# Kernel tuning notes

Measured on AMD Instinct MI355X. Metric: run time of the kernel, lower is better.

The kernel has to match this reference:

```python
import jax, jax.numpy as jnp
import numpy as np

N, B = 1024, 32
PEP_PAD, L, M, E, VOCAB = 3, 27, 34, 16, 26
CN, KS, OFFS = (128, 256, 256), (3, 5, 7), (2, 1, 0)
LIN = (512, 256)
BN_EPS = 1e-5


def _pe(length, d):
    pos = np.arange(length, dtype=np.float32)[:, None]
    div = np.exp(np.arange(0, d, 2, dtype=np.float32) * (-np.log(10000.0) / d))
    pe = np.zeros((length, d), np.float32)
    pe[:, 0::2] = np.sin(pos * div)
    pe[:, 1::2] = np.cos(pos * div)
    return jnp.asarray(pe)

PE_MHC = _pe(M, E)
PE_PEP = _pe(100, E)[: L - 2 * PEP_PAD]


def _bn(x, g, b):
    # inference-mode BatchNorm2d (running_mean=0, running_var=1)
    s = g / jnp.sqrt(1.0 + BN_EPS)
    return x * s[None, :, None, None] + b[None, :, None, None]


def _iconv(pep, mhc, W, b):
    # interaction conv: pep (N, Lin, E, S), mhc (N, M, E), W (C, K, M)
    # out[n,c,i,s] = sum_{k,m,e} W[c,k,m] * mhc[n,m,e] * pep[n,i+k,e,s] + b[c]
    K = W.shape[1]
    Kb = jnp.einsum('ckm,nme->ncke', W, mhc)  # per-sample kernel (N,C,K,E)
    Lout = pep.shape[1] - K + 1
    out = sum(jnp.einsum('nce,nies->ncis', Kb[:, :, k], pep[:, k:k + Lout]) for k in range(K))
    return out + b[None, :, None, None]


def _fwd(params, peptide_x, mhc_x, bags_size, inverse):
    (emb_pep, emb_mhc, convs_f, convs_r, lins_f, lins_r,
     w_att1, b_att1, w_att2, b_att2, w_out, b_out) = params
    masks = peptide_x[:, PEP_PAD:L - PEP_PAD] != 0              # (N, 21)
    mhc_e = emb_mhc[mhc_x] + PE_MHC                             # (N, 34, E)
    pep_e = emb_pep[peptide_x]
    pep_e = jnp.concatenate([pep_e[:, :PEP_PAD],
                             pep_e[:, PEP_PAD:L - PEP_PAD] + PE_PEP,
                             pep_e[:, L - PEP_PAD:]], axis=1)    # (N, 27, E)
    pep_c = pep_e[..., None]                                     # (N,27,E,1)
    pep_i = jnp.stack([pep_e[:, ::-1], pep_e], axis=-1)          # (N,27,E,2)

    def branch(pep, convs, inversion):
        outs = []
        for (W, bb, g, be), off in zip(convs, OFFS):
            Wk = W[:, ::-1] if inversion else W
            x = _iconv(pep[:, off:L - off], mhc_e, Wk, bb)
            outs.append(jax.nn.relu(_bn(x, g, be)))
        return jnp.concatenate(outs, axis=1)

    conv_out = branch(pep_c, convs_f, False)                     # (N, 640, 21, 1)
    conv_r = branch(pep_i, convs_r, True)                        # (N, 640, 21, 2)
    conv_r = jnp.concatenate([conv_r[..., 0:1][:, :, ::-1], conv_r[..., 1:2]], axis=-1)

    def mlp(x, lins):
        for Wl, bl, gl, bel in lins:
            x = jax.nn.relu(_bn(jnp.einsum('oc,nciw->noiw', Wl, x) + bl[None, :, None, None], gl, bel))
        return x

    conv_out = mlp(conv_out, lins_f)                             # (N, 256, 21, 1)
    conv_r = mlp(conv_r, lins_r)                                 # (N, 256, 21, 2)
    x = jnp.concatenate([conv_out, conv_r], axis=-1)             # (N, 256, 21, 3)
    m = masks[:, None, -x.shape[2]:, None]
    pool = jnp.max(jnp.where(m, x, -jnp.inf), axis=2, keepdims=True)  # (N,256,1,3)

    # attention MIL over variable-size bags (segment softmax)
    feat = pool.mean(axis=(2, 3))                                # (N, 256)
    a = (jnp.tanh(feat @ w_att1.T + b_att1) @ w_att2.T + b_att2)[:, 0]
    nb = bags_size.shape[0]
    seg = jnp.repeat(jnp.arange(nb), bags_size, total_repeat_length=feat.shape[0])
    amax = jax.lax.stop_gradient(jax.ops.segment_max(a, seg, num_segments=nb))
    ex = jnp.exp(a - amax[seg])
    att = ex / jax.ops.segment_sum(ex, seg, num_segments=nb)[seg]

    score = jax.nn.sigmoid(jnp.einsum('oc,nciw->noiw', w_out, pool) + b_out[None, :, None, None])  # (N,2,1,3)
    half = score[..., :2].sum(-1) * 0.5
    if inverse:
        s = jnp.stack([half, score[..., -1]], axis=-1)           # (N,2,1,2)
    else:
        s = jnp.stack([half, half], axis=-1)
    s = s.max(axis=-1)                                           # (N, 2, 1)
    if inverse:
        s = jax.ops.segment_sum(att[:, None, None] * s, seg, num_segments=nb)  # (B,2,1)
    else:
        s = s.sum(axis=-1) * 0.5
    s = jnp.clip(s, 0.0, 1.0)
    return s.reshape(s.shape[0], -1)                             # (B, 2)


def setup_inputs() -> dict:
    key = jax.random.key(0)
    ks = iter(jax.random.split(key, 64))
    nrm = lambda shape, std=0.02: jax.random.normal(next(ks), shape, jnp.float32) * std
    d = {}
    d['peptide_x'] = jax.random.randint(next(ks), (N, L), 1, VOCAB)
    d['mhc_x'] = jax.random.randint(next(ks), (N, M), 1, VOCAB)
    d['context_x'] = jax.random.randint(next(ks), (N, 12), 1, VOCAB)
    d['peptide_esm_x'] = jnp.zeros((N, 2, 10, 3), jnp.float32)
    d['bags_size'] = jnp.full((B,), N // B, jnp.int32)
    d['inverse'] = 1
    d['emb_pep'] = jax.random.uniform(next(ks), (VOCAB, E), jnp.float32, -0.1, 0.1)
    d['emb_mhc'] = jax.random.uniform(next(ks), (VOCAB, E), jnp.float32, -0.1, 0.1)
    for tag in ('cf', 'cr'):
        for j, (c, k) in enumerate(zip(CN, KS)):
            d[f'w_{tag}{j}'] = nrm((c, k, M), 0.05)
            d[f'b_{tag}{j}'] = jnp.zeros((c,), jnp.float32)
            d[f'g_{tag}{j}'] = 1.0 + nrm((c,), 0.002)
            d[f'be_{tag}{j}'] = jnp.zeros((c,), jnp.float32)
    dims = [sum(CN)] + list(LIN)
    for tag in ('lf', 'lr'):
        for j, (i_s, o_s) in enumerate(zip(dims[:-1], dims[1:])):
            d[f'w_{tag}{j}'] = nrm((o_s, i_s), 0.02)
            d[f'b_{tag}{j}'] = jnp.zeros((o_s,), jnp.float32)
            d[f'g_{tag}{j}'] = 1.0 + nrm((o_s,), 0.002)
            d[f'be_{tag}{j}'] = jnp.zeros((o_s,), jnp.float32)
    H = LIN[-1]
    d['w_att1'] = nrm((H, H)); d['b_att1'] = jnp.zeros((H,), jnp.float32)
    d['w_att2'] = nrm((1, H)); d['b_att2'] = jnp.zeros((1,), jnp.float32)
    d['w_out'] = nrm((2, H), 0.1); d['b_out'] = jnp.zeros((2,), jnp.float32)
    return d


def reference(peptide_x, mhc_x, context_x, peptide_esm_x, bags_size, inverse,
              emb_pep, emb_mhc,
              w_cf0, b_cf0, g_cf0, be_cf0, w_cf1, b_cf1, g_cf1, be_cf1, w_cf2, b_cf2, g_cf2, be_cf2,
              w_cr0, b_cr0, g_cr0, be_cr0, w_cr1, b_cr1, g_cr1, be_cr1, w_cr2, b_cr2, g_cr2, be_cr2,
              w_lf0, b_lf0, g_lf0, be_lf0, w_lf1, b_lf1, g_lf1, be_lf1,
              w_lr0, b_lr0, g_lr0, be_lr0, w_lr1, b_lr1, g_lr1, be_lr1,
              w_att1, b_att1, w_att2, b_att2, w_out, b_out):
    convs_f = [(w_cf0, b_cf0, g_cf0, be_cf0), (w_cf1, b_cf1, g_cf1, be_cf1), (w_cf2, b_cf2, g_cf2, be_cf2)]
    convs_r = [(w_cr0, b_cr0, g_cr0, be_cr0), (w_cr1, b_cr1, g_cr1, be_cr1), (w_cr2, b_cr2, g_cr2, be_cr2)]
    lins_f = [(w_lf0, b_lf0, g_lf0, be_lf0), (w_lf1, b_lf1, g_lf1, be_lf1)]
    lins_r = [(w_lr0, b_lr0, g_lr0, be_lr0), (w_lr1, b_lr1, g_lr1, be_lr1)]
    params = (emb_pep, emb_mhc, convs_f, convs_r, lins_f, lins_r,
              w_att1, b_att1, w_att2, b_att2, w_out, b_out)
    return _fwd(params, peptide_x, mhc_x, bags_size, int(inverse))
```

## Files before the change

### kernel.cpp

```cpp
#include <hip/hip_runtime.h>
#include <hip/hip_bf16.h>
#include <math.h>

#define NS   1024
#define LP   27
#define MMH  34
#define EE   16
#define LO   21
#define CT   640
#define H1   512
#define H2   256
#define LPAD 40
#define GROW (LP*LPAD)
#define SLOTROWS (NS*LO)
#define ALLROWS  (3*SLOTROWS)

typedef __attribute__((ext_vector_type(8))) short  s8v;
typedef __attribute__((ext_vector_type(4))) float  f4v;

#define PK2_SLOT 147456
#define PK2_J0   0
#define PK2_J1   16384
#define PK2_J2   73728
#define WMLP_FAM 458752
#define WMLP_B   327680
#define BMLP_FAM 768
#define BMLP_B   512

__device__ __forceinline__ ushort f2b(float v) {
    __hip_bfloat16 hb = __float2bfloat16(v);
    return *reinterpret_cast<ushort*>(&hb);
}

__device__ __forceinline__ float pe_val(int pos, int e) {
    int j = e >> 1;
    float div = expf(-1.1512925464970229f * (float)j);
    float ang = (float)pos * div;
    return (e & 1) ? cosf(ang) : sinf(ang);
}

struct PrepArgs {
    const int* pep_x; const int* mhc_x;
    const float* emb_pep; const float* emb_mhc;
    const float* cw[2][3]; const float* cb[2][3]; const float* cg[2][3]; const float* cbe[2][3];
    const float* mw[4]; const float* mb[4]; const float* mg[4]; const float* mbe[4];
    ushort* Gb; ushort* Wpack; float* bpack; ushort* Wmlp; float* bmlp;
};

__global__ __launch_bounds__(256) void k_prep(PrepArgs A) {
    int b = blockIdx.x, t = threadIdx.x;
    float rs = rsqrtf(1.0f + 1e-5f);
    if (b < NS) {
        __shared__ float ps[LP * 17];
        __shared__ float ms[MMH * 17];
        int n = b;
        for (int idx = t; idx < LP * EE; idx += 256) {
            int l = idx >> 4, e = idx & 15;
            float v = A.emb_pep[A.pep_x[n * LP + l] * EE + e];
            if (l >= 3 && l < 24) v += pe_val(l - 3, e);
            ps[l * 17 + e] = v;
        }
        for (int idx = t; idx < MMH * EE; idx += 256) {
            int m = idx >> 4, e = idx & 15;
            ms[m * 17 + e] = A.emb_mhc[A.mhc_x[n * MMH + m] * EE + e] + pe_val(m, e);
        }
        __syncthreads();
        for (int idx = t; idx < GROW; idx += 256) {
            int l = idx / LPAD, m = idx - l * LPAD;
            float s = 0.f;
            if (m < MMH) {
                #pragma unroll
                for (int e = 0; e < EE; ++e) s = fmaf(ps[l * 17 + e], ms[m * 17 + e], s);
            }
            A.Gb[(size_t)n * GROW + idx] = f2b(s);
        }
        if (n == 0 && t < 64) A.Gb[(size_t)NS * GROW + t] = 0;
    } else if (b < NS + 144) {
        const int KS_[3]  = {3, 5, 7};
        const int KCP_[3] = {128, 224, 288};
        const int NC_[3]  = {128, 256, 256};
        const int pkoff[3] = {PK2_J0, PK2_J1, PK2_J2};
        const int bpoff[3] = {0, 128, 384};
        int lin = b - NS;
        int s = lin / 48, rem = lin - s * 48, j = rem >> 4, z = rem & 15;
        int K = KS_[j], Kcp = KCP_[j], nc = NC_[j];
        int fam = (s == 0) ? 0 : 1;
        const float* w  = A.cw[fam][j];
        const float* g  = A.cg[fam][j];
        ushort* Wp = A.Wpack + s * PK2_SLOT + pkoff[j];
        int tot = nc * Kcp;
        for (int idx = z * 256 + t; idx < tot; idx += 16 * 256) {
            int c = idx / Kcp, col = idx - c * Kcp;
            int k = col / LPAD, m = col - k * LPAD;
            float v = 0.f;
            if (k < K && m < MMH) {
                int kk = (s == 2) ? (K - 1 - k) : k;
                v = w[((size_t)c * K + kk) * MMH + m] * (g[c] * rs);
            }
            Wp[idx] = f2b(v);
        }
        if (z == 0) {
            const float* bb = A.cb[fam][j];
            const float* be = A.cbe[fam][j];
            float* bp = A.bpack + s * CT + bpoff[j];
            for (int c = t; c < nc; c += 256)
                bp[c] = bb[c] * (g[c] * rs) + be[c];
        }
    } else {
        int lin = b - NS - 144;
        int task, rel, nb;
        if (lin < 40)      { task = 0; rel = lin;      nb = 40; }
        else if (lin < 56) { task = 1; rel = lin - 40; nb = 16; }
        else if (lin < 96) { task = 2; rel = lin - 56; nb = 40; }
        else               { task = 3; rel = lin - 96; nb = 16; }
        int fam = task >> 1, stage = task & 1;
        int Co = stage ? H2 : H1;
        int Ci = stage ? H1 : CT;
        const float* w  = A.mw[task];
        const float* g  = A.mg[task];
        ushort* Wb = A.Wmlp + fam * WMLP_FAM + stage * WMLP_B;
        int tot = Co * Ci;
        for (int idx = rel * 256 + t; idx < tot; idx += nb * 256) {
            int o = idx / Ci;
            Wb[idx] = f2b(w[idx] * (g[o] * rs));
        }
        if (rel == 0) {
            const float* bb = A.mb[task];
            const float* be = A.mbe[task];
            float* bp = A.bmlp + fam * BMLP_FAM + stage * BMLP_B;
            for (int o = t; o < Co; o += 256)
                bp[o] = bb[o] * (g[o] * rs) + be[o];
        }
    }
}

__global__ __launch_bounds__(256) void k_cmfma(
    const ushort* __restrict__ Gb, const ushort* __restrict__ Wpack,
    const float* __restrict__ bpack, ushort* __restrict__ Xb, int rowBase)
{
    const int kcpm[5] = {128, 224, 224, 288, 288};
    const int offm[5] = {2, 1, 1, 0, 0};
    const int o0m[5]  = {0, 0, 128, 0, 128};
    const int c0m[5]  = {0, 128, 128, 384, 384};
    const int wofm[5] = {PK2_J0, PK2_J1, PK2_J1, PK2_J2, PK2_J2};

    __shared__ ushort Al[128 * 40];
    __shared__ ushort Bl[128 * 40];
    int y = blockIdx.y;
    int Kcp = kcpm[y], off = offm[y], o0 = o0m[y];
    int r0g = rowBase + blockIdx.x * 128;
    int slot = r0g / SLOTROWS;
    const ushort* Wt = Wpack + slot * PK2_SLOT + wofm[y] + (size_t)o0 * Kcp;
    const float*  bp = bpack + slot * CT;
    int p0 = r0g - rowBase;

    int t = threadIdx.x, lane = t & 63, w = t >> 6;
    int r0 = (w >> 1) * 64, c0w = (w & 1) * 64;

    int row_a = t >> 2, seg = t & 3;
    int rg0 = r0g + row_a, rg1 = rg0 + 64;
    int rr0 = rg0 - slot * SLOTROWS, rr1 = rg1 - slot * SLOTROWS;
    size_t wb0 = (size_t)(rr0 / LO) * GROW + (off + rr0 % LO) * LPAD;
    size_t wb1 = (size_t)(rr1 / LO) * GROW + (off + rr1 % LO) * LPAD;

    f4v acc[4][4];
    #pragma unroll
    for (int m = 0; m < 4; ++m)
        #pragma unroll
        for (int n = 0; n < 4; ++n)
            acc[m][n] = (f4v){0.f, 0.f, 0.f, 0.f};

    int nkt = Kcp >> 5;
    for (int kt = 0; kt < nkt; ++kt) {
        int k0 = kt << 5;
        __syncthreads();
        *(s8v*)&Al[row_a * 40 + seg * 8]        = *(const s8v*)&Gb[wb0 + k0 + seg * 8];
        *(s8v*)&Al[(row_a + 64) * 40 + seg * 8] = *(const s8v*)&Gb[wb1 + k0 + seg * 8];
        *(s8v*)&Bl[row_a * 40 + seg * 8]        = *(const s8v*)&Wt[(size_t)row_a * Kcp + k0 + seg * 8];
        *(s8v*)&Bl[(row_a + 64) * 40 + seg * 8] = *(const s8v*)&Wt[(size_t)(row_a + 64) * Kcp + k0 + seg * 8];
        __syncthreads();
        s8v a[4], b[4];
        #pragma unroll
        for (int m = 0; m < 4; ++m)
            a[m] = *(const s8v*)&Al[(r0 + m * 16 + (lane & 15)) * 40 + (lane >> 4) * 8];
        #pragma unroll
        for (int n = 0; n < 4; ++n)
            b[n] = *(const s8v*)&Bl[(c0w + n * 16 + (lane & 15)) * 40 + (lane >> 4) * 8];
        #pragma unroll
        for (int m = 0; m < 4; ++m)
            #pragma unroll
            for (int n = 0; n < 4; ++n)
                acc[m][n] = __builtin_amdgcn_mfma_f32_16x16x32_bf16(a[m], b[n], acc[m][n], 0, 0, 0);
    }

    int cl = lane & 15, rq = lane >> 4;
    #pragma unroll
    for (int m = 0; m < 4; ++m) {
        #pragma unroll
        for (int n = 0; n < 4; ++n) {
            int oc = c0m[y] + o0 + c0w + n * 16 + cl;
            float bv = bp[oc];
            #pragma unroll
            for (int j = 0; j < 4; ++j) {
                int p = p0 + r0 + m * 16 + rq * 4 + j;
                Xb[(size_t)p * CT + oc] = f2b(fmaxf(acc[m][n][j] + bv, 0.f));
            }
        }
    }
}

template<int OUTB>
__global__ __launch_bounds__(256) void k_mgemm(
    const ushort* __restrict__ Xin, int Cin,
    const ushort* __restrict__ Wbase, const float* __restrict__ bbase,
    int woff, int boff,
    ushort* __restrict__ Yb, float* __restrict__ Yf, int Cout, int rowBase)
{
    __shared__ ushort Al[128 * 40];
    __shared__ ushort Bl[128 * 40];
    int t = threadIdx.x;
    int p0g = rowBase + blockIdx.x * 128;
    int fam = (p0g < SLOTROWS) ? 0 : 1;
    const ushort* Wb = Wbase + (size_t)fam * WMLP_FAM + woff;
    const float*  bp = bbase + fam * BMLP_FAM + boff;
    int p0 = p0g - rowBase, o0 = blockIdx.y * 128;
    int lane = t & 63, w = t >> 6;
    int r0 = (w >> 1) * 64, c0 = (w & 1) * 64;

    f4v acc[4][4];
    #pragma unroll
    for (int m = 0; m < 4; ++m)
        #pragma unroll
        for (int n = 0; n < 4; ++n)
            acc[m][n] = (f4v){0.f, 0.f, 0.f, 0.f};

    int nkt = Cin >> 5;
    for (int kt = 0; kt < nkt; ++kt) {
        int k0 = kt << 5;
        __syncthreads();
        #pragma unroll
        for (int h = 0; h < 2; ++h) {
            int L = t + h * 256;
            int row = L >> 2, seg = L & 3;
            *(s8v*)&Al[row * 40 + seg * 8] =
                *(const s8v*)&Xin[(size_t)(p0 + row) * Cin + k0 + seg * 8];
            *(s8v*)&Bl[row * 40 + seg * 8] =
                *(const s8v*)&Wb[(size_t)(o0 + row) * Cin + k0 + seg * 8];
        }
        __syncthreads();
        s8v a[4], b[4];
        #pragma unroll
        for (int m = 0; m < 4; ++m)
            a[m] = *(const s8v*)&Al[(r0 + m * 16 + (lane & 15)) * 40 + (lane >> 4) * 8];
        #pragma unroll
        for (int n = 0; n < 4; ++n)
            b[n] = *(const s8v*)&Bl[(c0 + n * 16 + (lane & 15)) * 40 + (lane >> 4) * 8];
        #pragma unroll
        for (int m = 0; m < 4; ++m)
            #pragma unroll
            for (int n = 0; n < 4; ++n)
                acc[m][n] = __builtin_amdgcn_mfma_f32_16x16x32_bf16(a[m], b[n], acc[m][n], 0, 0, 0);
    }

    int cl = lane & 15, rq = lane >> 4;
    #pragma unroll
    for (int m = 0; m < 4; ++m) {
        #pragma unroll
        for (int n = 0; n < 4; ++n) {
            int o = o0 + c0 + n * 16 + cl;
            float bv = bp[o];
            #pragma unroll
            for (int j = 0; j < 4; ++j) {
                int p = p0 + r0 + m * 16 + rq * 4 + j;
                float v = fmaxf(acc[m][n][j] + bv, 0.f);
                if (OUTB) {
                    Yb[(size_t)p * Cout + o] = f2b(v);
                } else {
                    Yf[(size_t)p * Cout + o] = v;
                }
            }
        }
    }
}

__global__ __launch_bounds__(128) void k_pool(
    const float* __restrict__ Zc, const int* __restrict__ pep_x,
    float* __restrict__ pool, int rowBase)
{
    int sl = blockIdx.x;
    int sg = rowBase / LO + sl;
    int slot = sg / NS, n = sg - slot * NS;
    int c = blockIdx.y * 128 + threadIdx.x;
    float m = -INFINITY;
    for (int i = 0; i < LO; ++i)
        if (pep_x[n * LP + 3 + i] != 0)
            m = fmaxf(m, Zc[(size_t)(sl * LO + i) * H2 + c]);
    pool[(size_t)n * (3 * H2) + slot * H2 + c] = m;
}

__global__ __launch_bounds__(256) void k_poolhead(
    const float* __restrict__ pool,
    const float* __restrict__ w_att1, const float* __restrict__ b_att1,
    const float* __restrict__ w_att2, const float* __restrict__ b_att2,
    const float* __restrict__ w_out, const float* __restrict__ b_out,
    float* __restrict__ a_out, float* __restrict__ s2_out)
{
    int n = blockIdx.x, c = threadIdx.x;
    __shared__ float feat_s[H2];
    __shared__ float red[7][H2];
    __shared__ float sc_s[6];

    float mx[3];
    #pragma unroll
    for (int w = 0; w < 3; ++w)
        mx[w] = pool[(size_t)n * (3 * H2) + w * H2 + c];

    float fv = (mx[0] + mx[1] + mx[2]) * (1.f / 3.f);
    feat_s[c] = fv;
    #pragma unroll
    for (int o = 0; o < 2; ++o)
        #pragma unroll
        for (int w = 0; w < 3; ++w)
            red[o * 3 + w][c] = w_out[o * H2 + c] * mx[w];
    __syncthreads();

    float hacc = 0.f;
    for (int cc = 0; cc < H2; ++cc)
        hacc = fmaf(w_att1[(size_t)c * H2 + cc], feat_s[cc], hacc);
    float h = tanhf(hacc + b_att1[c]);
    red[6][c] = h * w_att2[c];
    __syncthreads();

    for (int s = 128; s > 0; s >>= 1) {
        if (c < s) {
            #pragma unroll
            for (int jj = 0; jj < 7; ++jj) red[jj][c] += red[jj][c + s];
        }
        __syncthreads();
    }
    if (c == 0) a_out[n] = red[6][0] + b_att2[0];
    if (c < 6) {
        float x = red[c][0] + b_out[c / 3];
        sc_s[c] = 1.f / (1.f + expf(-x));
    }
    __syncthreads();
    if (c < 2) {
        float half = 0.5f * (sc_s[c * 3 + 0] + sc_s[c * 3 + 1]);
        s2_out[n * 2 + c] = fmaxf(half, sc_s[c * 3 + 2]);
    }
}

__global__ __launch_bounds__(1024) void k_final(
    const float* __restrict__ a_in, const float* __restrict__ s2_in,
    const int* __restrict__ bags, float* __restrict__ out)
{
    __shared__ float a_s[NS], s0_s[NS], s1_s[NS];
    __shared__ int off_s[33];
    int t = threadIdx.x;
    a_s[t]  = a_in[t];
    s0_s[t] = s2_in[t * 2 + 0];
    s1_s[t] = s2_in[t * 2 + 1];
    if (t == 0) {
        off_s[0] = 0;
        for (int g = 0; g < 32; ++g) off_s[g + 1] = off_s[g] + bags[g];
    }
    __syncthreads();
    if (t < 32) {
        int st = off_s[t], en = off_s[t + 1];
        float mxv = -INFINITY;
        for (int n = st; n < en; ++n) mxv = fmaxf(mxv, a_s[n]);
        float se = 0.f;
        for (int n = st; n < en; ++n) se += expf(a_s[n] - mxv);
        float inv = 1.f / se;
        float o0 = 0.f, o1 = 0.f;
        for (int n = st; n < en; ++n) {
            float w = expf(a_s[n] - mxv) * inv;
            o0 += w * s0_s[n];
            o1 += w * s1_s[n];
        }
        out[t * 2 + 0] = fminf(fmaxf(o0, 0.f), 1.f);
        out[t * 2 + 1] = fminf(fmaxf(o1, 0.f), 1.f);
    }
}

extern "C" void kernel_launch(void* const* d_in, const int* in_sizes, int n_in,
                              void* d_out, int out_size, void* d_ws, size_t ws_size,
                              hipStream_t stream) {
    const int* pep_x = (const int*)d_in[0];
    const int* mhc_x = (const int*)d_in[1];
    const int* bags  = (const int*)d_in[4];

    char* wsb = (char*)d_ws;
    float*  pool   = (float*) (wsb + 0);
    float*  a_buf  = (float*) (wsb + 3145728);
    float*  s2_buf = (float*) (wsb + 3149824);
    ushort* Wpack  = (ushort*)(wsb + 3158016);
    float*  bpack  = (float*) (wsb + 4042752);
    ushort* Wmlp   = (ushort*)(wsb + 4050432);
    float*  bmlp   = (float*) (wsb + 5885440);
    ushort* Gb     = (ushort*)(wsb + 5891584);
    const size_t XB_B = 8103552;

    size_t fullNeed = XB_B + (size_t)ALLROWS * (1280 + 1024 + 1024);
    int chunkSlots = (fullNeed <= ws_size) ? 3 : 1;
    int RC = chunkSlots * SLOTROWS;
    ushort* Xb = (ushort*)(wsb + XB_B);
    ushort* Yb = (ushort*)((char*)Xb + (size_t)RC * 1280);
    float*  Zc = (float*) ((char*)Yb + (size_t)RC * 1024);

    PrepArgs pa;
    pa.pep_x = pep_x; pa.mhc_x = mhc_x;
    pa.emb_pep = (const float*)d_in[6];
    pa.emb_mhc = (const float*)d_in[7];
    for (int j = 0; j < 3; ++j) {
        pa.cw[0][j]  = (const float*)d_in[8 + 4 * j];
        pa.cb[0][j]  = (const float*)d_in[9 + 4 * j];
        pa.cg[0][j]  = (const float*)d_in[10 + 4 * j];
        pa.cbe[0][j] = (const float*)d_in[11 + 4 * j];
        pa.cw[1][j]  = (const float*)d_in[20 + 4 * j];
        pa.cb[1][j]  = (const float*)d_in[21 + 4 * j];
        pa.cg[1][j]  = (const float*)d_in[22 + 4 * j];
        pa.cbe[1][j] = (const float*)d_in[23 + 4 * j];
    }
    for (int task = 0; task < 4; ++task) {
        int base = 32 + task * 4;
        pa.mw[task]  = (const float*)d_in[base + 0];
        pa.mb[task]  = (const float*)d_in[base + 1];
        pa.mg[task]  = (const float*)d_in[base + 2];
        pa.mbe[task] = (const float*)d_in[base + 3];
    }
    pa.Gb = Gb; pa.Wpack = Wpack; pa.bpack = bpack; pa.Wmlp = Wmlp; pa.bmlp = bmlp;

    k_prep<<<dim3(NS + 144 + 112), dim3(256), 0, stream>>>(pa);

    for (int rowBase = 0; rowBase < ALLROWS; rowBase += RC) {
        int nRB = RC / 128;
        k_cmfma<<<dim3(nRB, 5), dim3(256), 0, stream>>>(Gb, Wpack, bpack, Xb, rowBase);
        k_mgemm<1><<<dim3(nRB, H1 / 128), dim3(256), 0, stream>>>(
            Xb, CT, Wmlp, bmlp, 0, 0, Yb, nullptr, H1, rowBase);
        k_mgemm<0><<<dim3(nRB, H2 / 128), dim3(256), 0, stream>>>(
            Yb, H1, Wmlp, bmlp, WMLP_B, BMLP_B, nullptr, Zc, H2, rowBase);
        k_pool<<<dim3(RC / LO, H2 / 128), dim3(128), 0, stream>>>(
            Zc, pep_x, pool, rowBase);
    }

    k_poolhead<<<dim3(NS), dim3(256), 0, stream>>>(
        pool,
        (const float*)d_in[48], (const float*)d_in[49], (const float*)d_in[50], (const float*)d_in[51],
        (const float*)d_in[52], (const float*)d_in[53],
        a_buf, s2_buf);

    k_final<<<dim3(1), dim3(1024), 0, stream>>>(a_buf, s2_buf, bags, (float*)d_out);
}
```

Baseline: 231.2 us.

## Fuse masked max-pool into second MLP GEMM and stage GEMM outputs through LDS

Drops the separate pooling kernel and the fp32 Zc intermediate. The second MLP GEMM now does a masked max over sequence positions in shared memory and combines partial maxima across row tiles with integer atomicMax into a pool buffer that k_prep zeroes. The conv and MLP GEMM epilogues stage results in LDS so global stores become 16-byte vectorized writes, and the MLP GEMMs use a K-tile of 64. The grid order is swapped so column tiles sharing an A row-tile run next to each other. The atomicMax trick only holds for non-negative ReLU outputs and adds atomics plus extra shared memory per block.

```diff
diff --git a/kernel.cpp b/kernel.cpp
--- a/kernel.cpp
+++ b/kernel.cpp
@@ -44,7 +44,7 @@
     const float* emb_pep; const float* emb_mhc;
     const float* cw[2][3]; const float* cb[2][3]; const float* cg[2][3]; const float* cbe[2][3];
     const float* mw[4]; const float* mb[4]; const float* mg[4]; const float* mbe[4];
-    ushort* Gb; ushort* Wpack; float* bpack; ushort* Wmlp; float* bmlp;
+    ushort* Gb; ushort* Wpack; float* bpack; ushort* Wmlp; float* bmlp; int* poolI;
 };
 
 __global__ __launch_bounds__(256) void k_prep(PrepArgs A) {
@@ -106,7 +106,7 @@
             for (int c = t; c < nc; c += 256)
                 bp[c] = bb[c] * (g[c] * rs) + be[c];
         }
-    } else {
+    } else if (b < NS + 144 + 112) {
         int lin = b - NS - 144;
         int task, rel, nb;
         if (lin < 40)      { task = 0; rel = lin;      nb = 40; }
@@ -131,6 +131,11 @@
             for (int o = t; o < Co; o += 256)
                 bp[o] = bb[o] * (g[o] * rs) + be[o];
         }
+    } else {
+        int base = (b - NS - 144 - 112) * 8192;
+        #pragma unroll
+        for (int q = 0; q < 32; ++q)
+            A.poolI[base + q * 256 + t] = 0;
     }
 }
 
@@ -144,15 +149,17 @@
     const int c0m[5]  = {0, 128, 128, 384, 384};
     const int wofm[5] = {PK2_J0, PK2_J1, PK2_J1, PK2_J2, PK2_J2};
 
-    __shared__ ushort Al[128 * 40];
-    __shared__ ushort Bl[128 * 40];
-    int y = blockIdx.y;
+    __shared__ ushort smC[17408];
+    ushort* Al = smC;
+    ushort* Bl = smC + 5120;
+    int y = blockIdx.x;
     int Kcp = kcpm[y], off = offm[y], o0 = o0m[y];
-    int r0g = rowBase + blockIdx.x * 128;
+    int c0X = c0m[y] + o0;
+    int r0g = rowBase + blockIdx.y * 128;
     int slot = r0g / SLOTROWS;
     const ushort* Wt = Wpack + slot * PK2_SLOT + wofm[y] + (size_t)o0 * Kcp;
     const float*  bp = bpack + slot * CT;
-    int p0 = r0g - rowBase;
+    int p0 = blockIdx.y * 128;
 
     int t = threadIdx.x, lane = t & 63, w = t >> 6;
     int r0 = (w >> 1) * 64, c0w = (w & 1) * 64;
@@ -194,36 +201,41 @@
     }
 
     int cl = lane & 15, rq = lane >> 4;
-    #pragma unroll
-    for (int m = 0; m < 4; ++m) {
+    __syncthreads();
+    #pragma unroll
+    for (int m = 0; m < 4; ++m)
         #pragma unroll
         for (int n = 0; n < 4; ++n) {
-            int oc = c0m[y] + o0 + c0w + n * 16 + cl;
-            float bv = bp[oc];
-            #pragma unroll
-            for (int j = 0; j < 4; ++j) {
-                int p = p0 + r0 + m * 16 + rq * 4 + j;
-                Xb[(size_t)p * CT + oc] = f2b(fmaxf(acc[m][n][j] + bv, 0.f));
-            }
-        }
-    }
-}
-
-template<int OUTB>
-__global__ __launch_bounds__(256) void k_mgemm(
-    const ushort* __restrict__ Xin, int Cin,
+            int ocr = c0w + n * 16 + cl;
+            float bv = bp[c0X + ocr];
+            #pragma unroll
+            for (int j = 0; j < 4; ++j)
+                smC[(r0 + m * 16 + rq * 4 + j) * 136 + ocr] = f2b(fmaxf(acc[m][n][j] + bv, 0.f));
+        }
+    __syncthreads();
+    int ci = t & 15;
+    #pragma unroll
+    for (int it = 0; it < 8; ++it) {
+        int row = (t >> 4) + it * 16;
+        *(s8v*)&Xb[(size_t)(p0 + row) * CT + c0X + ci * 8] = *(const s8v*)&smC[row * 136 + ci * 8];
+    }
+}
+
+__global__ __launch_bounds__(256) void k_mgemmA(
+    const ushort* __restrict__ Xin,
     const ushort* __restrict__ Wbase, const float* __restrict__ bbase,
-    int woff, int boff,
-    ushort* __restrict__ Yb, float* __restrict__ Yf, int Cout, int rowBase)
+    ushort* __restrict__ Yb, int rowBase)
 {
-    __shared__ ushort Al[128 * 40];
-    __shared__ ushort Bl[128 * 40];
+    __shared__ ushort smA[18432];
+    ushort* Al = smA;
+    ushort* Bl = smA + 9216;
     int t = threadIdx.x;
-    int p0g = rowBase + blockIdx.x * 128;
-    int fam = (p0g < SLOTROWS) ? 0 : 1;
-    const ushort* Wb = Wbase + (size_t)fam * WMLP_FAM + woff;
-    const float*  bp = bbase + fam * BMLP_FAM + boff;
-    int p0 = p0g - rowBase, o0 = blockIdx.y * 128;
+    int o0 = blockIdx.x * 128;
+    int p0 = blockIdx.y * 128;
+    int g0 = rowBase + p0;
+    int fam = (g0 < SLOTROWS) ? 0 : 1;
+    const ushort* Wb = Wbase + (size_t)fam * WMLP_FAM;
+    const float*  bp = bbase + fam * BMLP_FAM;
     int lane = t & 63, w = t >> 6;
     int r0 = (w >> 1) * 64, c0 = (w & 1) * 64;
 
@@ -234,68 +246,148 @@
         for (int n = 0; n < 4; ++n)
             acc[m][n] = (f4v){0.f, 0.f, 0.f, 0.f};
 
-    int nkt = Cin >> 5;
-    for (int kt = 0; kt < nkt; ++kt) {
-        int k0 = kt << 5;
-        __syncthreads();
-        #pragma unroll
-        for (int h = 0; h < 2; ++h) {
-            int L = t + h * 256;
-            int row = L >> 2, seg = L & 3;
-            *(s8v*)&Al[row * 40 + seg * 8] =
-                *(const s8v*)&Xin[(size_t)(p0 + row) * Cin + k0 + seg * 8];
-            *(s8v*)&Bl[row * 40 + seg * 8] =
-                *(const s8v*)&Wb[(size_t)(o0 + row) * Cin + k0 + seg * 8];
-        }
-        __syncthreads();
-        s8v a[4], b[4];
-        #pragma unroll
-        for (int m = 0; m < 4; ++m)
-            a[m] = *(const s8v*)&Al[(r0 + m * 16 + (lane & 15)) * 40 + (lane >> 4) * 8];
+    for (int kt = 0; kt < CT / 64; ++kt) {
+        int k0 = kt << 6;
+        __syncthreads();
+        #pragma unroll
+        for (int it = 0; it < 4; ++it) {
+            int idx = t + it * 256;
+            int row = idx >> 3, sg = idx & 7;
+            *(s8v*)&Al[row * 72 + sg * 8] = *(const s8v*)&Xin[(size_t)(p0 + row) * CT + k0 + sg * 8];
+            *(s8v*)&Bl[row * 72 + sg * 8] = *(const s8v*)&Wb[(size_t)(o0 + row) * CT + k0 + sg * 8];
+        }
+        __syncthreads();
+        #pragma unroll
+        for (int ks = 0; ks < 2; ++ks) {
+            int kc = ks * 32 + (lane >> 4) * 8;
+            s8v a[4], b[4];
+            #pragma unroll
+            for (int m = 0; m < 4; ++m)
+                a[m] = *(const s8v*)&Al[(r0 + m * 16 + (lane & 15)) * 72 + kc];
+            #pragma unroll
+            for (int n = 0; n < 4; ++n)
+                b[n] = *(const s8v*)&Bl[(c0 + n * 16 + (lane & 15)) * 72 + kc];
+            #pragma unroll
+            for (int m = 0; m < 4; ++m)
+                #pragma unroll
+                for (int n = 0; n < 4; ++n)
+                    acc[m][n] = __builtin_amdgcn_mfma_f32_16x16x32_bf16(a[m], b[n], acc[m][n], 0, 0, 0);
+        }
+    }
+
+    int cl = lane & 15, rq = lane >> 4;
+    __syncthreads();
+    #pragma unroll
+    for (int m = 0; m < 4; ++m)
+        #pragma unroll
+        for (int n = 0; n < 4; ++n) {
+            int ocr = c0 + n * 16 + cl;
+            float bv = bp[o0 + ocr];
+            #pragma unroll
+            for (int j = 0; j < 4; ++j)
+                smA[(r0 + m * 16 + rq * 4 + j) * 136 + ocr] = f2b(fmaxf(acc[m][n][j] + bv, 0.f));
+        }
+    __syncthreads();
+    int ci = t & 15;
+    #pragma unroll
+    for (int it = 0; it < 8; ++it) {
+        int row = (t >> 4) + it * 16;
+        *(s8v*)&Yb[(size_t)(p0 + row) * H1 + o0 + ci * 8] = *(const s8v*)&smA[row * 136 + ci * 8];
+    }
+}
+
+__global__ __launch_bounds__(256) void k_mgemmB(
+    const ushort* __restrict__ Yin,
+    const ushort* __restrict__ Wbase, const float* __restrict__ bbase,
+    const int* __restrict__ pep_x, int* __restrict__ poolI, int rowBase)
+{
+    __shared__ float zbuf[128 * 129];
+    __shared__ int mvalid[128];
+    ushort* Al = (ushort*)zbuf;
+    ushort* Bl = Al + 9216;
+    int t = threadIdx.x;
+    int o0 = blockIdx.x * 128;
+    int p0 = blockIdx.y * 128;
+    int g0 = rowBase + p0;
+    int slot = g0 / SLOTROWS;
+    int gs0 = g0 - slot * SLOTROWS;
+    int fam = (slot == 0) ? 0 : 1;
+    const ushort* Wb = Wbase + (size_t)fam * WMLP_FAM + WMLP_B;
+    const float*  bp = bbase + fam * BMLP_FAM + BMLP_B;
+    int lane = t & 63, w = t >> 6;
+    int r0 = (w >> 1) * 64, c0 = (w & 1) * 64;
+
+    f4v acc[4][4];
+    #pragma unroll
+    for (int m = 0; m < 4; ++m)
         #pragma unroll
         for (int n = 0; n < 4; ++n)
-            b[n] = *(const s8v*)&Bl[(c0 + n * 16 + (lane & 15)) * 40 + (lane >> 4) * 8];
-        #pragma unroll
-        for (int m = 0; m < 4; ++m)
+            acc[m][n] = (f4v){0.f, 0.f, 0.f, 0.f};
+
+    for (int kt = 0; kt < H1 / 64; ++kt) {
+        int k0 = kt << 6;
+        __syncthreads();
+        #pragma unroll
+        for (int it = 0; it < 4; ++it) {
+            int idx = t + it * 256;
+            int row = idx >> 3, sg = idx & 7;
+            *(s8v*)&Al[row * 72 + sg * 8] = *(const s8v*)&Yin[(size_t)(p0 + row) * H1 + k0 + sg * 8];
+            *(s8v*)&Bl[row * 72 + sg * 8] = *(const s8v*)&Wb[(size_t)(o0 + row) * H1 + k0 + sg * 8];
+        }
+        __syncthreads();
+        #pragma unroll
+        for (int ks = 0; ks < 2; ++ks) {
+            int kc = ks * 32 + (lane >> 4) * 8;
+            s8v a[4], b[4];
+            #pragma unroll
+            for (int m = 0; m < 4; ++m)
+                a[m] = *(const s8v*)&Al[(r0 + m * 16 + (lane & 15)) * 72 + kc];
             #pragma unroll
             for (int n = 0; n < 4; ++n)
-                acc[m][n] = __builtin_amdgcn_mfma_f32_16x16x32_bf16(a[m], b[n], acc[m][n], 0, 0, 0);
+                b[n] = *(const s8v*)&Bl[(c0 + n * 16 + (lane & 15)) * 72 + kc];
+            #pragma unroll
+            for (int m = 0; m < 4; ++m)
+                #pragma unroll
+                for (int n = 0; n < 4; ++n)
+                    acc[m][n] = __builtin_amdgcn_mfma_f32_16x16x32_bf16(a[m], b[n], acc[m][n], 0, 0, 0);
+        }
     }
 
     int cl = lane & 15, rq = lane >> 4;
-    #pragma unroll
-    for (int m = 0; m < 4; ++m) {
+    __syncthreads();
+    if (t < 128) {
+        int gs = gs0 + t;
+        int n = gs / LO, i = gs - n * LO;
+        mvalid[t] = (pep_x[n * LP + 3 + i] != 0) ? 1 : 0;
+    }
+    #pragma unroll
+    for (int m = 0; m < 4; ++m)
         #pragma unroll
         for (int n = 0; n < 4; ++n) {
-            int o = o0 + c0 + n * 16 + cl;
-            float bv = bp[o];
-            #pragma unroll
-            for (int j = 0; j < 4; ++j) {
-                int p = p0 + r0 + m * 16 + rq * 4 + j;
-                float v = fmaxf(acc[m][n][j] + bv, 0.f);
-                if (OUTB) {
-                    Yb[(size_t)p * Cout + o] = f2b(v);
-                } else {
-                    Yf[(size_t)p * Cout + o] = v;
-                }
-            }
-        }
-    }
-}
-
-__global__ __launch_bounds__(128) void k_pool(
-    const float* __restrict__ Zc, const int* __restrict__ pep_x,
-    float* __restrict__ pool, int rowBase)
-{
-    int sl = blockIdx.x;
-    int sg = rowBase / LO + sl;
-    int slot = sg / NS, n = sg - slot * NS;
-    int c = blockIdx.y * 128 + threadIdx.x;
-    float m = -INFINITY;
-    for (int i = 0; i < LO; ++i)
-        if (pep_x[n * LP + 3 + i] != 0)
-            m = fmaxf(m, Zc[(size_t)(sl * LO + i) * H2 + c]);
-    pool[(size_t)n * (3 * H2) + slot * H2 + c] = m;
+            int ocr = c0 + n * 16 + cl;
+            float bv = bp[o0 + ocr];
+            #pragma unroll
+            for (int j = 0; j < 4; ++j)
+                zbuf[(r0 + m * 16 + rq * 4 + j) * 129 + ocr] = fmaxf(acc[m][n][j] + bv, 0.f);
+        }
+    __syncthreads();
+
+    int col = t & 127, half = t >> 7;
+    int colg = o0 + col;
+    int rs = half * 64;
+    int gs = gs0 + rs;
+    int n = gs / LO, i = gs - n * LO;
+    float cur = -1.f;
+    for (int r = rs; r < rs + 64; ++r) {
+        if (mvalid[r]) cur = fmaxf(cur, zbuf[r * 129 + col]);
+        if (++i == LO) {
+            if (cur >= 0.f)
+                atomicMax(&poolI[n * (3 * H2) + slot * H2 + colg], __float_as_int(cur));
+            cur = -1.f; ++n; i = 0;
+        }
+    }
+    if (cur >= 0.f)
+        atomicMax(&poolI[n * (3 * H2) + slot * H2 + colg], __float_as_int(cur));
 }
 
 __global__ __launch_bounds__(256) void k_poolhead(
@@ -392,6 +484,7 @@
 
     char* wsb = (char*)d_ws;
     float*  pool   = (float*) (wsb + 0);
+    int*    poolI  = (int*)   (wsb + 0);
     float*  a_buf  = (float*) (wsb + 3145728);
     float*  s2_buf = (float*) (wsb + 3149824);
     ushort* Wpack  = (ushort*)(wsb + 3158016);
@@ -401,12 +494,11 @@
     ushort* Gb     = (ushort*)(wsb + 5891584);
     const size_t XB_B = 8103552;
 
-    size_t fullNeed = XB_B + (size_t)ALLROWS * (1280 + 1024 + 1024);
+    size_t fullNeed = XB_B + (size_t)ALLROWS * (1280 + 1024);
     int chunkSlots = (fullNeed <= ws_size) ? 3 : 1;
     int RC = chunkSlots * SLOTROWS;
     ushort* Xb = (ushort*)(wsb + XB_B);
     ushort* Yb = (ushort*)((char*)Xb + (size_t)RC * 1280);
-    float*  Zc = (float*) ((char*)Yb + (size_t)RC * 1024);
 
     PrepArgs pa;
     pa.pep_x = pep_x; pa.mhc_x = mhc_x;
@@ -430,18 +522,15 @@
         pa.mbe[task] = (const float*)d_in[base + 3];
     }
     pa.Gb = Gb; pa.Wpack = Wpack; pa.bpack = bpack; pa.Wmlp = Wmlp; pa.bmlp = bmlp;
-
-    k_prep<<<dim3(NS + 144 + 112), dim3(256), 0, stream>>>(pa);
+    pa.poolI = poolI;
+
+    k_prep<<<dim3(NS + 144 + 112 + 96), dim3(256), 0, stream>>>(pa);
 
     for (int rowBase = 0; rowBase < ALLROWS; rowBase += RC) {
         int nRB = RC / 128;
-        k_cmfma<<<dim3(nRB, 5), dim3(256), 0, stream>>>(Gb, Wpack, bpack, Xb, rowBase);
-        k_mgemm<1><<<dim3(nRB, H1 / 128), dim3(256), 0, stream>>>(
-            Xb, CT, Wmlp, bmlp, 0, 0, Yb, nullptr, H1, rowBase);
-        k_mgemm<0><<<dim3(nRB, H2 / 128), dim3(256), 0, stream>>>(
-            Yb, H1, Wmlp, bmlp, WMLP_B, BMLP_B, nullptr, Zc, H2, rowBase);
-        k_pool<<<dim3(RC / LO, H2 / 128), dim3(128), 0, stream>>>(
-            Zc, pep_x, pool, rowBase);
+        k_cmfma<<<dim3(5, nRB), dim3(256), 0, stream>>>(Gb, Wpack, bpack, Xb, rowBase);
+        k_mgemmA<<<dim3(H1 / 128, nRB), dim3(256), 0, stream>>>(Xb, Wmlp, bmlp, Yb, rowBase);
+        k_mgemmB<<<dim3(H2 / 128, nRB), dim3(256), 0, stream>>>(Yb, Wmlp, bmlp, pep_x, poolI, rowBase);
     }
 
     k_poolhead<<<dim3(NS), dim3(256), 0, stream>>>(
```

Result: faster. 207.1 us (-10.4%).
